# Kernel optimization log

Hardware: AMD Instinct MI355X
Metric: run time of the kernel (lower is better)

## Reference

```python
import jax, jax.numpy as jnp
import numpy as np

H = 256          # hidden_size
W2V = 256        # word2vec embedding dim
FEAT = 4096      # video frame feature dim
T_ENC = 80       # video_frame


def _lstm_cell(x, h, c, W_ih, W_hh, b_ih, b_hh):
    # PyTorch LSTMCell gate order: i, f, g, o
    gates = x @ W_ih.T + b_ih + h @ W_hh.T + b_hh
    i, f, g, o = jnp.split(gates, 4, axis=-1)
    c_new = jax.nn.sigmoid(f) * c + jax.nn.sigmoid(i) * jnp.tanh(g)
    h_new = jax.nn.sigmoid(o) * jnp.tanh(c_new)
    return h_new, c_new


def setup_inputs() -> dict:
    key = jax.random.key(0)
    ks = jax.random.split(key, 14)
    B, L, V = 256, 40, 6000
    sc = 0.02
    inp = {
        "feat": jax.random.normal(ks[0], (B, T_ENC, FEAT), jnp.float32),
        "caption": jax.random.normal(ks[1], (B, L, W2V), jnp.float32),
        "caption_one_hot": jax.random.normal(ks[2], (B, L, V), jnp.float32),
        # lstm1: input 4096 -> hidden 256
        "W_ih1": jax.random.normal(ks[3], (4 * H, FEAT), jnp.float32) * sc,
        "W_hh1": jax.random.normal(ks[4], (4 * H, H), jnp.float32) * sc,
        "b_ih1": jnp.zeros((4 * H,), jnp.float32),
        "b_hh1": jnp.zeros((4 * H,), jnp.float32),
        # lstm2: input hidden+word2vec = 512 -> hidden 256
        "W_ih2": jax.random.normal(ks[5], (4 * H, H + W2V), jnp.float32) * sc,
        "W_hh2": jax.random.normal(ks[6], (4 * H, H), jnp.float32) * sc,
        "b_ih2": jnp.zeros((4 * H,), jnp.float32),
        "b_hh2": jnp.zeros((4 * H,), jnp.float32),
        # output projection hidden -> vocab
        "W_out": jax.random.normal(ks[7], (V, H), jnp.float32) * sc,
        "b_out": jnp.zeros((V,), jnp.float32),
    }
    return inp


def reference(feat, caption, caption_one_hot,
              W_ih1, W_hh1, b_ih1, b_hh1,
              W_ih2, W_hh2, b_ih2, b_hh2,
              W_out, b_out):
    B = feat.shape[0]
    L = caption.shape[1]  # decoder_length
    pad1 = jnp.zeros((B, FEAT), feat.dtype)
    pad2 = jnp.zeros((B, H), feat.dtype)
    h1 = jnp.zeros((B, H), feat.dtype)
    c1 = jnp.zeros((B, H), feat.dtype)
    h2 = jnp.zeros((B, H), feat.dtype)
    c2 = jnp.zeros((B, H), feat.dtype)

    # ---- encoding phase: 80 video frames ----
    def enc_step(carry, x_t):
        h1, c1, h2, c2 = carry
        h1, c1 = _lstm_cell(x_t, h1, c1, W_ih1, W_hh1, b_ih1, b_hh1)
        h2, c2 = _lstm_cell(jnp.concatenate([pad2, h1], axis=1), h2, c2,
                            W_ih2, W_hh2, b_ih2, b_hh2)
        return (h1, c1, h2, c2), None

    carry, _ = jax.lax.scan(enc_step, (h1, c1, h2, c2),
                            feat.transpose(1, 0, 2))  # [T,B,4096]

    # ---- decoding phase: decoder_length-1 steps with per-step CE ----
    targets = jnp.argmax(caption_one_hot, axis=-1)      # [B,L] int
    dec_in = caption[:, :L - 1, :].transpose(1, 0, 2)   # [L-1,B,W2V]
    dec_tgt = targets[:, 1:].T                          # [L-1,B]

    def dec_step(carry, xt):
        h1, c1, h2, c2 = carry
        cap_t, tgt_t = xt
        h1, c1 = _lstm_cell(pad1, h1, c1, W_ih1, W_hh1, b_ih1, b_hh1)
        h2, c2 = _lstm_cell(jnp.concatenate([cap_t, h1], axis=1), h2, c2,
                            W_ih2, W_hh2, b_ih2, b_hh2)
        logits = h2 @ W_out.T + b_out                   # [B,V]
        lsm = jax.nn.log_softmax(logits, axis=-1)
        nll = -jnp.take_along_axis(lsm, tgt_t[:, None], axis=1)[:, 0]
        # torch: total_loss += sum(word_loss)/batch_size  ==  mean over batch
        return (h1, c1, h2, c2), jnp.mean(nll)

    _, step_losses = jax.lax.scan(dec_step, carry, (dec_in, dec_tgt))
    return jnp.sum(step_losses)
```

## Files before the change

kernel.cpp:

```cpp
#include <hip/hip_runtime.h>


typedef unsigned short u16;
typedef __attribute__((ext_vector_type(8))) short s8v;
typedef __attribute__((ext_vector_type(4))) float f4v;

#define VOC   6000
#define VOCP  6016
#define CHUNK_M 3328

__device__ __forceinline__ u16 f2b(float f) {
  unsigned u = __float_as_uint(f);
  unsigned r = (u + 0x7fffu + ((u >> 16) & 1u)) >> 16;
  return (u16)r;
}
__device__ __forceinline__ float sigm(float x) { return 1.f / (1.f + __expf(-x)); }
__device__ __forceinline__ float tanh_f(float x) {
  float e = __expf(-2.f * fabsf(x));
  float t = (1.f - e) / (1.f + e);
  return x >= 0.f ? t : -t;
}

__global__ void pack_bf16(u16* __restrict__ dst, int dld, int doff,
                          const float* __restrict__ src, int sld, int soff,
                          int Wc, int R, int Rsrc) {
  int i = blockIdx.x * 256 + threadIdx.x;
  if (i >= Wc * R) return;
  int r = i / Wc, c = i - r * Wc;
  float v = (r < Rsrc) ? src[(size_t)r * sld + soff + c] : 0.f;
  dst[(size_t)r * dld + doff + c] = f2b(v);
}

__global__ void bias_setup(const float* __restrict__ bi1, const float* __restrict__ bh1,
                           const float* __restrict__ bi2, const float* __restrict__ bh2,
                           const float* __restrict__ bo,
                           float* __restrict__ b1s, float* __restrict__ b2s,
                           float* __restrict__ bop) {
  int i = blockIdx.x * 256 + threadIdx.x;
  if (i < 1024) { b1s[i] = bi1[i] + bh1[i]; b2s[i] = bi2[i] + bh2[i]; }
  if (i < VOCP) bop[i] = (i < VOC) ? bo[i] : 0.f;
}

__global__ __launch_bounds__(256) void argmax_kernel(const float* __restrict__ coh,
                                                     int* __restrict__ tgt) {
  const int d = blockIdx.x >> 8;
  const int b = blockIdx.x & 255;
  const float* row = coh + ((size_t)b * 40 + (d + 1)) * VOC;
  float best = -3.4e38f; int bi = 0;
  for (int n = threadIdx.x; n < VOC; n += 256) {
    float v = row[n];
    if (v > best) { best = v; bi = n; }
  }
#pragma unroll
  for (int o = 1; o < 64; o <<= 1) {
    float ov = __shfl_xor(best, o);
    int   oi = __shfl_xor(bi, o);
    if (ov > best || (ov == best && oi < bi)) { best = ov; bi = oi; }
  }
  __shared__ float sv[4]; __shared__ int si[4];
  if ((threadIdx.x & 63) == 0) { sv[threadIdx.x >> 6] = best; si[threadIdx.x >> 6] = bi; }
  __syncthreads();
  if (threadIdx.x == 0) {
    for (int i = 1; i < 4; ++i)
      if (sv[i] > best || (sv[i] == best && si[i] < bi)) { best = sv[i]; bi = si[i]; }
    tgt[blockIdx.x] = bi;
  }
}

__global__ __launch_bounds__(256) void gemm_bf16(
    const float* __restrict__ A, const u16* __restrict__ Bw,
    const float* __restrict__ bias, float* __restrict__ C,
    int K, int lda, int ldc)
{
  const int n0 = blockIdx.x * 128;
  const int m0 = blockIdx.y * 128;
  const int tid = threadIdx.x;
  const int lane = tid & 63;
  const int wid = tid >> 6;
  const int wm = wid >> 1, wn = wid & 1;
  const int fr = lane & 15;
  const int fk = (lane >> 4) * 8;
  const int sr = tid >> 1;
  const int sc = (tid & 1) * 32;

  __shared__ u16 As[128][72];
  __shared__ u16 Bs[128][72];
  f4v acc[4][4] = {};

  for (int k0 = 0; k0 < K; k0 += 64) {
    const float* ap = A + (size_t)(m0 + sr) * lda + (k0 + sc);
    const u16*   bp = Bw + (size_t)(n0 + sr) * K + (k0 + sc);
    float af[32];
#pragma unroll
    for (int v = 0; v < 8; ++v) {
      float4 t4 = *reinterpret_cast<const float4*>(ap + v * 4);
      af[v*4+0] = t4.x; af[v*4+1] = t4.y; af[v*4+2] = t4.z; af[v*4+3] = t4.w;
    }
    int4 bv[4];
#pragma unroll
    for (int v = 0; v < 4; ++v) bv[v] = *reinterpret_cast<const int4*>(bp + v * 8);
    __syncthreads();
#pragma unroll
    for (int v = 0; v < 4; ++v) {
      int w0 = (int)((unsigned)f2b(af[v*8+0]) | ((unsigned)f2b(af[v*8+1]) << 16));
      int w1 = (int)((unsigned)f2b(af[v*8+2]) | ((unsigned)f2b(af[v*8+3]) << 16));
      int w2 = (int)((unsigned)f2b(af[v*8+4]) | ((unsigned)f2b(af[v*8+5]) << 16));
      int w3 = (int)((unsigned)f2b(af[v*8+6]) | ((unsigned)f2b(af[v*8+7]) << 16));
      *reinterpret_cast<int4*>(&As[sr][sc + v*8]) = make_int4(w0, w1, w2, w3);
      *reinterpret_cast<int4*>(&Bs[sr][sc + v*8]) = bv[v];
    }
    __syncthreads();
#pragma unroll
    for (int ks = 0; ks < 2; ++ks) {
      const int kb = ks * 32 + fk;
      s8v a[4], b[4];
#pragma unroll
      for (int i = 0; i < 4; ++i)
        a[i] = *reinterpret_cast<const s8v*>(&As[wm*64 + i*16 + fr][kb]);
#pragma unroll
      for (int j = 0; j < 4; ++j)
        b[j] = *reinterpret_cast<const s8v*>(&Bs[wn*64 + j*16 + fr][kb]);
#pragma unroll
      for (int i = 0; i < 4; ++i)
#pragma unroll
        for (int j = 0; j < 4; ++j)
          acc[i][j] = __builtin_amdgcn_mfma_f32_16x16x32_bf16(a[i], b[j], acc[i][j], 0, 0, 0);
    }
  }
#pragma unroll
  for (int j = 0; j < 4; ++j) {
    const int n = n0 + wn*64 + j*16 + fr;
    const float bz = bias[n];
#pragma unroll
    for (int i = 0; i < 4; ++i) {
      const int rb = m0 + wm*64 + i*16 + (lane >> 4) * 4;
#pragma unroll
      for (int r = 0; r < 4; ++r)
        C[(size_t)(rb + r) * ldc + n] = acc[i][j][r] + bz;
    }
  }
}

__global__ __launch_bounds__(256) void step_kernel(
    int t,
    const float* __restrict__ X1,
    const float* __restrict__ Xc,
    const float* __restrict__ b1sum, const float* __restrict__ b2sum,
    const u16* __restrict__ Whh1,
    const u16* __restrict__ Wcat2,
    u16* __restrict__ hcat, float* __restrict__ c1, float* __restrict__ c2,
    float* __restrict__ H2dec)
{
  const int lane = threadIdx.x & 63;
  const int w = threadIdx.x >> 6;
  const int fr = lane & 15;
  const int fk = (lane >> 4) * 8;
  const u16* hr = hcat + (size_t)((t + 1) & 1) * (256 * 512);
  u16*       hw = hcat + (size_t)(t & 1) * (256 * 512);

  if (blockIdx.x < 64) {
    if (t > 118) return;
    const int bm = blockIdx.x >> 4;
    const int bh = blockIdx.x & 15;
    const int rowbase = bm * 64 + w * 16;
    f4v acc[4] = {};
    const u16* arow = hr + (size_t)(rowbase + fr) * 512;
#pragma unroll
    for (int kk = 0; kk < 8; ++kk) {
      const int kb = kk * 32 + fk;
      s8v a = *reinterpret_cast<const s8v*>(arow + kb);
#pragma unroll
      for (int q = 0; q < 4; ++q) {
        s8v wv = *reinterpret_cast<const s8v*>(Whh1 + (size_t)(q*256 + bh*16 + fr) * 256 + kb);
        acc[q] = __builtin_amdgcn_mfma_f32_16x16x32_bf16(a, wv, acc[q], 0, 0, 0);
      }
    }
    const int hd = bh * 16 + fr;
    float xb0 = 0, xb1 = 0, xb2 = 0, xb3 = 0;
    if (t >= 80) { xb0 = b1sum[hd]; xb1 = b1sum[256+hd]; xb2 = b1sum[512+hd]; xb3 = b1sum[768+hd]; }
#pragma unroll
    for (int r = 0; r < 4; ++r) {
      const int bat = rowbase + (lane >> 4) * 4 + r;
      float g0 = acc[0][r], g1 = acc[1][r], g2 = acc[2][r], g3 = acc[3][r];
      if (t < 80) {
        const float* xp = X1 + ((size_t)bat * 80 + t) * 1024;
        g0 += xp[hd]; g1 += xp[256+hd]; g2 += xp[512+hd]; g3 += xp[768+hd];
      } else { g0 += xb0; g1 += xb1; g2 += xb2; g3 += xb3; }
      const int ci = bat * 256 + hd;
      float co = c1[ci];
      float ii = sigm(g0), ff = sigm(g1), gg = tanh_f(g2), oo = sigm(g3);
      float cn = ff * co + ii * gg;
      float h = oo * tanh_f(cn);
      c1[ci] = cn;
      hw[(size_t)bat * 512 + hd] = f2b(h);
    }
  } else {
    if (t < 1) return;
    const int s = t - 1;
    const int bb = blockIdx.x - 64;
    const int bm = bb >> 4;
    const int bh = bb & 15;
    const int rowbase = bm * 64 + w * 16;
    f4v acc[4] = {};
    const u16* arow = hr + (size_t)(rowbase + fr) * 512;
#pragma unroll
    for (int kk = 0; kk < 16; ++kk) {
      const int kb = kk * 32 + fk;
      s8v a = *reinterpret_cast<const s8v*>(arow + kb);
#pragma unroll
      for (int q = 0; q < 4; ++q) {
        s8v wv = *reinterpret_cast<const s8v*>(Wcat2 + (size_t)(q*256 + bh*16 + fr) * 512 + kb);
        acc[q] = __builtin_amdgcn_mfma_f32_16x16x32_bf16(a, wv, acc[q], 0, 0, 0);
      }
    }
    const int hd = bh * 16 + fr;
    float xb0 = 0, xb1 = 0, xb2 = 0, xb3 = 0;
    if (s < 80) { xb0 = b2sum[hd]; xb1 = b2sum[256+hd]; xb2 = b2sum[512+hd]; xb3 = b2sum[768+hd]; }
#pragma unroll
    for (int r = 0; r < 4; ++r) {
      const int bat = rowbase + (lane >> 4) * 4 + r;
      float g0 = acc[0][r], g1 = acc[1][r], g2 = acc[2][r], g3 = acc[3][r];
      if (s >= 80) {
        const float* xp = Xc + ((size_t)bat * 40 + (s - 80)) * 1024;
        g0 += xp[hd]; g1 += xp[256+hd]; g2 += xp[512+hd]; g3 += xp[768+hd];
      } else { g0 += xb0; g1 += xb1; g2 += xb2; g3 += xb3; }
      const int ci = bat * 256 + hd;
      float co = c2[ci];
      float ii = sigm(g0), ff = sigm(g1), gg = tanh_f(g2), oo = sigm(g3);
      float cn = ff * co + ii * gg;
      float h = oo * tanh_f(cn);
      c2[ci] = cn;
      hw[(size_t)bat * 512 + 256 + hd] = f2b(h);
      if (s >= 80) H2dec[((size_t)(s - 80) * 256 + bat) * 256 + hd] = h;
    }
  }
}

__global__ __launch_bounds__(256) void nll_kernel(const float* __restrict__ logits,
                                                  const int* __restrict__ tgt,
                                                  float* __restrict__ rowloss, int rg0) {
  const int rl = blockIdx.x;
  const float* row = logits + (size_t)rl * VOCP;
  const int tid = threadIdx.x;
  float mx = -3.4e38f;
  for (int n = tid; n < VOC; n += 256) mx = fmaxf(mx, row[n]);
#pragma unroll
  for (int o = 1; o < 64; o <<= 1) mx = fmaxf(mx, __shfl_xor(mx, o));
  __shared__ float s1[4];
  if ((tid & 63) == 0) s1[tid >> 6] = mx;
  __syncthreads();
  mx = fmaxf(fmaxf(s1[0], s1[1]), fmaxf(s1[2], s1[3]));
  float sm = 0.f;
  for (int n = tid; n < VOC; n += 256) sm += __expf(row[n] - mx);
#pragma unroll
  for (int o = 1; o < 64; o <<= 1) sm += __shfl_xor(sm, o);
  __shared__ float s2[4];
  if ((tid & 63) == 0) s2[tid >> 6] = sm;
  __syncthreads();
  if (tid == 0) {
    float tot = s2[0] + s2[1] + s2[2] + s2[3];
    rowloss[rg0 + rl] = mx + __logf(tot) - row[tgt[rg0 + rl]];
  }
}

__global__ __launch_bounds__(256) void final_kernel(const float* __restrict__ rowloss,
                                                    float* __restrict__ out) {
  float s = 0.f;
  for (int n = threadIdx.x; n < 9984; n += 256) s += rowloss[n];
#pragma unroll
  for (int o = 1; o < 64; o <<= 1) s += __shfl_xor(s, o);
  __shared__ float sr[4];
  if ((threadIdx.x & 63) == 0) sr[threadIdx.x >> 6] = s;
  __syncthreads();
  if (threadIdx.x == 0) out[0] = (sr[0] + sr[1] + sr[2] + sr[3]) * (1.f / 256.f);
}

extern "C" void kernel_launch(void* const* d_in, const int* in_sizes, int n_in,
                              void* d_out, int out_size, void* d_ws, size_t ws_size,
                              hipStream_t stream) {
  const float* feat    = (const float*)d_in[0];
  const float* caption = (const float*)d_in[1];
  const float* coh     = (const float*)d_in[2];
  const float* W_ih1   = (const float*)d_in[3];
  const float* W_hh1   = (const float*)d_in[4];
  const float* b_ih1   = (const float*)d_in[5];
  const float* b_hh1   = (const float*)d_in[6];
  const float* W_ih2   = (const float*)d_in[7];
  const float* W_hh2   = (const float*)d_in[8];
  const float* b_ih2   = (const float*)d_in[9];
  const float* b_hh2   = (const float*)d_in[10];
  const float* W_out   = (const float*)d_in[11];
  const float* b_out   = (const float*)d_in[12];

  char* p = (char*)d_ws;
  auto take = [&](size_t bytes) { char* r = p; p += (bytes + 255) & ~(size_t)255; return r; };
  float* X1     = (float*)take(20480ull * 1024 * 4);
  float* Xc     = (float*)take(10240ull * 1024 * 4);
  float* H2dec  = (float*)take(9984ull * 256 * 4);
  float* logits = (float*)take((size_t)CHUNK_M * VOCP * 4);
  u16* Wih1b  = (u16*)take(1024ull * 4096 * 2);
  u16* Whh1b  = (u16*)take(1024ull * 256 * 2);
  u16* Wih2ab = (u16*)take(1024ull * 256 * 2);
  u16* Wcat2b = (u16*)take(1024ull * 512 * 2);
  u16* Woutb  = (u16*)take((size_t)VOCP * 256 * 2);
  u16* hcat   = (u16*)take(2ull * 256 * 512 * 2);
  float* c1   = (float*)take(256ull * 256 * 4);
  float* c2   = (float*)take(256ull * 256 * 4);
  float* b1sum = (float*)take(1024 * 4);
  float* b2sum = (float*)take(1024 * 4);
  float* boutp = (float*)take(VOCP * 4);
  int*   tgt   = (int*)take(9984 * 4);
  float* rowloss = (float*)take(9984 * 4);

  hipMemsetAsync(hcat, 0, 2ull * 256 * 512 * 2 + 2ull * 256 * 256 * 4, stream);
  bias_setup<<<dim3(24), dim3(256), 0, stream>>>(b_ih1, b_hh1, b_ih2, b_hh2, b_out,
                                                 b1sum, b2sum, boutp);
  auto pack = [&](u16* dst, int dld, int doff, const float* src, int sld, int soff,
                  int Wc, int R, int Rs) {
    int tot = Wc * R;
    pack_bf16<<<dim3((tot + 255) / 256), dim3(256), 0, stream>>>(dst, dld, doff, src, sld, soff,
                                                                 Wc, R, Rs);
  };
  pack(Wih1b, 4096, 0, W_ih1, 4096, 0, 4096, 1024, 1024);
  pack(Whh1b, 256, 0, W_hh1, 256, 0, 256, 1024, 1024);
  pack(Wih2ab, 256, 0, W_ih2, 512, 0, 256, 1024, 1024);
  pack(Wcat2b, 512, 0, W_ih2, 512, 256, 256, 1024, 1024);
  pack(Wcat2b, 512, 256, W_hh2, 256, 0, 256, 1024, 1024);
  pack(Woutb, 256, 0, W_out, 256, 0, 256, VOCP, VOC);

  argmax_kernel<<<dim3(39 * 256), dim3(256), 0, stream>>>(coh, tgt);

  gemm_bf16<<<dim3(8, 160), dim3(256), 0, stream>>>(feat, Wih1b, b1sum, X1, 4096, 4096, 1024);
  gemm_bf16<<<dim3(8, 80), dim3(256), 0, stream>>>(caption, Wih2ab, b2sum, Xc, 256, 256, 1024);

  for (int t = 0; t <= 119; ++t)
    step_kernel<<<dim3(128), dim3(256), 0, stream>>>(t, X1, Xc, b1sum, b2sum,
                                                     Whh1b, Wcat2b, hcat, c1, c2, H2dec);

  for (int ch = 0; ch < 3; ++ch) {
    gemm_bf16<<<dim3(VOCP / 128, CHUNK_M / 128), dim3(256), 0, stream>>>(
        H2dec + (size_t)ch * CHUNK_M * 256, Woutb, boutp, logits, 256, 256, VOCP);
    nll_kernel<<<dim3(CHUNK_M), dim3(256), 0, stream>>>(logits, tgt, rowloss, ch * CHUNK_M);
  }
  final_kernel<<<dim3(1), dim3(256), 0, stream>>>(rowloss, (float*)d_out);
}
```

Measured before the change: 2.717 ms.

## Persistent recurrent kernel with grid barrier, bf16 intermediates, larger GEMM tiles

Replaces the 120 per-step launches with one persistent kernel. It keeps recurrent weights and cell state in registers and synchronises steps through a global atomic barrier. Feature and caption inputs are converted to bf16 in a separate pass, and the GEMM becomes a 128x256 tile with register prefetch of the next K slice. X1, Xc and H2dec are now stored in bf16, and argmax/nll use vectorised loads. This cuts launch overhead and memory traffic, but the spin barrier needs all 128 blocks co-resident, and the extra bf16 rounding may shift numerics.

```diff
diff --git a/kernel.cpp b/kernel.cpp
--- a/kernel.cpp
+++ b/kernel.cpp
@@ -6,19 +6,36 @@
 typedef __attribute__((ext_vector_type(4))) float f4v;
 
 #define VOC   6000
-#define VOCP  6016
+#define VOCP  6144
 #define CHUNK_M 3328
 
 __device__ __forceinline__ u16 f2b(float f) {
   unsigned u = __float_as_uint(f);
   unsigned r = (u + 0x7fffu + ((u >> 16) & 1u)) >> 16;
   return (u16)r;
+}
+__device__ __forceinline__ float b2f(u16 u) {
+  return __uint_as_float(((unsigned)u) << 16);
 }
 __device__ __forceinline__ float sigm(float x) { return 1.f / (1.f + __expf(-x)); }
 __device__ __forceinline__ float tanh_f(float x) {
   float e = __expf(-2.f * fabsf(x));
   float t = (1.f - e) / (1.f + e);
   return x >= 0.f ? t : -t;
+}
+
+__global__ __launch_bounds__(256) void conv_f2b(const float* __restrict__ src,
+                                                u16* __restrict__ dst, long n) {
+  long stride = (long)gridDim.x * 2048;
+  for (long i = ((long)blockIdx.x * 256 + threadIdx.x) * 8; i < n; i += stride) {
+    float4 a = *(const float4*)(src + i);
+    float4 b = *(const float4*)(src + i + 4);
+    unsigned w0 = (unsigned)f2b(a.x) | ((unsigned)f2b(a.y) << 16);
+    unsigned w1 = (unsigned)f2b(a.z) | ((unsigned)f2b(a.w) << 16);
+    unsigned w2 = (unsigned)f2b(b.x) | ((unsigned)f2b(b.y) << 16);
+    unsigned w3 = (unsigned)f2b(b.z) | ((unsigned)f2b(b.w) << 16);
+    *(int4*)(dst + i) = make_int4((int)w0, (int)w1, (int)w2, (int)w3);
+  }
 }
 
 __global__ void pack_bf16(u16* __restrict__ dst, int dld, int doff,
@@ -45,11 +62,14 @@
                                                      int* __restrict__ tgt) {
   const int d = blockIdx.x >> 8;
   const int b = blockIdx.x & 255;
-  const float* row = coh + ((size_t)b * 40 + (d + 1)) * VOC;
+  const float4* row = (const float4*)(coh + ((size_t)b * 40 + (d + 1)) * VOC);
   float best = -3.4e38f; int bi = 0;
-  for (int n = threadIdx.x; n < VOC; n += 256) {
-    float v = row[n];
-    if (v > best) { best = v; bi = n; }
+  for (int v = threadIdx.x; v < VOC / 4; v += 256) {
+    float4 x = row[v];
+    float vals[4] = {x.x, x.y, x.z, x.w};
+#pragma unroll
+    for (int j = 0; j < 4; ++j)
+      if (vals[j] > best) { best = vals[j]; bi = v * 4 + j; }
   }
 #pragma unroll
   for (int o = 1; o < 64; o <<= 1) {
@@ -67,172 +87,225 @@
   }
 }
 
-__global__ __launch_bounds__(256) void gemm_bf16(
-    const float* __restrict__ A, const u16* __restrict__ Bw,
-    const float* __restrict__ bias, float* __restrict__ C,
-    int K, int lda, int ldc)
+template <int OB>
+__global__ __launch_bounds__(256) void gemm_bb(
+    const u16* __restrict__ A, const u16* __restrict__ Bw,
+    const float* __restrict__ bias, void* __restrict__ Cout,
+    int K, int ldc)
 {
-  const int n0 = blockIdx.x * 128;
-  const int m0 = blockIdx.y * 128;
+  const int m0 = blockIdx.x * 128;
+  const int n0 = blockIdx.y * 256;
   const int tid = threadIdx.x;
   const int lane = tid & 63;
   const int wid = tid >> 6;
   const int wm = wid >> 1, wn = wid & 1;
   const int fr = lane & 15;
   const int fk = (lane >> 4) * 8;
-  const int sr = tid >> 1;
-  const int sc = (tid & 1) * 32;
+  const int rq = lane >> 4;
 
   __shared__ u16 As[128][72];
-  __shared__ u16 Bs[128][72];
-  f4v acc[4][4] = {};
-
+  __shared__ u16 Bs[256][72];
+  f4v acc[4][8] = {};
+
+  const int ar = tid >> 1, ac = (tid & 1) * 32;
+  int4 av[4], bv[8];
+  {
+    const u16* ap = A + (size_t)(m0 + ar) * K + ac;
+    const u16* bp = Bw + (size_t)(n0 + tid) * K;
+#pragma unroll
+    for (int v = 0; v < 4; ++v) av[v] = *(const int4*)(ap + v * 8);
+#pragma unroll
+    for (int v = 0; v < 8; ++v) bv[v] = *(const int4*)(bp + v * 8);
+  }
+#pragma unroll 1
   for (int k0 = 0; k0 < K; k0 += 64) {
-    const float* ap = A + (size_t)(m0 + sr) * lda + (k0 + sc);
-    const u16*   bp = Bw + (size_t)(n0 + sr) * K + (k0 + sc);
-    float af[32];
-#pragma unroll
-    for (int v = 0; v < 8; ++v) {
-      float4 t4 = *reinterpret_cast<const float4*>(ap + v * 4);
-      af[v*4+0] = t4.x; af[v*4+1] = t4.y; af[v*4+2] = t4.z; af[v*4+3] = t4.w;
-    }
-    int4 bv[4];
-#pragma unroll
-    for (int v = 0; v < 4; ++v) bv[v] = *reinterpret_cast<const int4*>(bp + v * 8);
     __syncthreads();
 #pragma unroll
-    for (int v = 0; v < 4; ++v) {
-      int w0 = (int)((unsigned)f2b(af[v*8+0]) | ((unsigned)f2b(af[v*8+1]) << 16));
-      int w1 = (int)((unsigned)f2b(af[v*8+2]) | ((unsigned)f2b(af[v*8+3]) << 16));
-      int w2 = (int)((unsigned)f2b(af[v*8+4]) | ((unsigned)f2b(af[v*8+5]) << 16));
-      int w3 = (int)((unsigned)f2b(af[v*8+6]) | ((unsigned)f2b(af[v*8+7]) << 16));
-      *reinterpret_cast<int4*>(&As[sr][sc + v*8]) = make_int4(w0, w1, w2, w3);
-      *reinterpret_cast<int4*>(&Bs[sr][sc + v*8]) = bv[v];
-    }
+    for (int v = 0; v < 4; ++v) *(int4*)&As[ar][ac + v * 8] = av[v];
+#pragma unroll
+    for (int v = 0; v < 8; ++v) *(int4*)&Bs[tid][v * 8] = bv[v];
     __syncthreads();
+    if (k0 + 64 < K) {
+      const u16* ap = A + (size_t)(m0 + ar) * K + k0 + 64 + ac;
+      const u16* bp = Bw + (size_t)(n0 + tid) * K + k0 + 64;
+#pragma unroll
+      for (int v = 0; v < 4; ++v) av[v] = *(const int4*)(ap + v * 8);
+#pragma unroll
+      for (int v = 0; v < 8; ++v) bv[v] = *(const int4*)(bp + v * 8);
+    }
 #pragma unroll
     for (int ks = 0; ks < 2; ++ks) {
       const int kb = ks * 32 + fk;
-      s8v a[4], b[4];
+      s8v a[4], b[8];
+#pragma unroll
+      for (int i = 0; i < 4; ++i) a[i] = *(const s8v*)&As[wm * 64 + i * 16 + fr][kb];
+#pragma unroll
+      for (int j = 0; j < 8; ++j) b[j] = *(const s8v*)&Bs[wn * 128 + j * 16 + fr][kb];
 #pragma unroll
       for (int i = 0; i < 4; ++i)
-        a[i] = *reinterpret_cast<const s8v*>(&As[wm*64 + i*16 + fr][kb]);
-#pragma unroll
-      for (int j = 0; j < 4; ++j)
-        b[j] = *reinterpret_cast<const s8v*>(&Bs[wn*64 + j*16 + fr][kb]);
-#pragma unroll
-      for (int i = 0; i < 4; ++i)
-#pragma unroll
-        for (int j = 0; j < 4; ++j)
+#pragma unroll
+        for (int j = 0; j < 8; ++j)
           acc[i][j] = __builtin_amdgcn_mfma_f32_16x16x32_bf16(a[i], b[j], acc[i][j], 0, 0, 0);
     }
   }
 #pragma unroll
-  for (int j = 0; j < 4; ++j) {
-    const int n = n0 + wn*64 + j*16 + fr;
+  for (int j = 0; j < 8; ++j) {
+    const int n = n0 + wn * 128 + j * 16 + fr;
     const float bz = bias[n];
 #pragma unroll
     for (int i = 0; i < 4; ++i) {
-      const int rb = m0 + wm*64 + i*16 + (lane >> 4) * 4;
-#pragma unroll
-      for (int r = 0; r < 4; ++r)
-        C[(size_t)(rb + r) * ldc + n] = acc[i][j][r] + bz;
-    }
-  }
-}
-
-__global__ __launch_bounds__(256) void step_kernel(
-    int t,
-    const float* __restrict__ X1,
-    const float* __restrict__ Xc,
+      const int rb = m0 + wm * 64 + i * 16 + rq * 4;
+#pragma unroll
+      for (int r = 0; r < 4; ++r) {
+        float vout = acc[i][j][r] + bz;
+        if (OB) ((u16*)Cout)[(size_t)(rb + r) * ldc + n] = f2b(vout);
+        else    ((float*)Cout)[(size_t)(rb + r) * ldc + n] = vout;
+      }
+    }
+  }
+}
+
+__device__ __forceinline__ void gbar(unsigned* bar, unsigned target) {
+  __syncthreads();
+  if (threadIdx.x == 0) {
+    __threadfence();
+    __hip_atomic_fetch_add(bar, 1u, __ATOMIC_RELEASE, __HIP_MEMORY_SCOPE_AGENT);
+    while (__hip_atomic_load(bar, __ATOMIC_RELAXED, __HIP_MEMORY_SCOPE_AGENT) < target) {
+      __builtin_amdgcn_s_sleep(2);
+    }
+    __threadfence();
+  }
+  __syncthreads();
+}
+
+__global__ __launch_bounds__(256, 1) void recur_kernel(
+    const u16* __restrict__ X1,
+    const u16* __restrict__ Xc,
     const float* __restrict__ b1sum, const float* __restrict__ b2sum,
     const u16* __restrict__ Whh1,
     const u16* __restrict__ Wcat2,
-    u16* __restrict__ hcat, float* __restrict__ c1, float* __restrict__ c2,
-    float* __restrict__ H2dec)
+    u16* __restrict__ hcat,
+    u16* __restrict__ H2dec,
+    unsigned* __restrict__ bar)
 {
-  const int lane = threadIdx.x & 63;
-  const int w = threadIdx.x >> 6;
+  const int tid = threadIdx.x;
+  const int lane = tid & 63;
+  const int w = tid >> 6;
   const int fr = lane & 15;
   const int fk = (lane >> 4) * 8;
-  const u16* hr = hcat + (size_t)((t + 1) & 1) * (256 * 512);
-  u16*       hw = hcat + (size_t)(t & 1) * (256 * 512);
-
-  if (blockIdx.x < 64) {
-    if (t > 118) return;
-    const int bm = blockIdx.x >> 4;
-    const int bh = blockIdx.x & 15;
-    const int rowbase = bm * 64 + w * 16;
-    f4v acc[4] = {};
-    const u16* arow = hr + (size_t)(rowbase + fr) * 512;
-#pragma unroll
-    for (int kk = 0; kk < 8; ++kk) {
-      const int kb = kk * 32 + fk;
-      s8v a = *reinterpret_cast<const s8v*>(arow + kb);
-#pragma unroll
-      for (int q = 0; q < 4; ++q) {
-        s8v wv = *reinterpret_cast<const s8v*>(Whh1 + (size_t)(q*256 + bh*16 + fr) * 256 + kb);
-        acc[q] = __builtin_amdgcn_mfma_f32_16x16x32_bf16(a, wv, acc[q], 0, 0, 0);
+  const int rq = lane >> 4;
+  const bool p2 = blockIdx.x >= 64;
+  const int bb = p2 ? (int)blockIdx.x - 64 : (int)blockIdx.x;
+  const int bm = bb >> 4;
+  const int bh = bb & 15;
+  const int hd = bh * 16 + fr;
+  const int rowA = bm * 64 + w * 16 + fr;
+  const int batbase = bm * 64 + w * 16 + rq * 4;
+
+  s8v wv[64];
+  float br[4];
+  if (!p2) {
+#pragma unroll
+    for (int q = 0; q < 4; ++q) {
+      br[q] = b1sum[q * 256 + hd];
+#pragma unroll
+      for (int kk = 0; kk < 8; ++kk)
+        wv[q * 8 + kk] =
+            *(const s8v*)(Whh1 + (size_t)(q * 256 + bh * 16 + fr) * 256 + kk * 32 + fk);
+    }
+  } else {
+#pragma unroll
+    for (int q = 0; q < 4; ++q) {
+      br[q] = b2sum[q * 256 + hd];
+#pragma unroll
+      for (int kk = 0; kk < 16; ++kk)
+        wv[q * 16 + kk] =
+            *(const s8v*)(Wcat2 + (size_t)(q * 256 + bh * 16 + fr) * 512 + kk * 32 + fk);
+    }
+  }
+  float creg[4] = {0.f, 0.f, 0.f, 0.f};
+
+#pragma unroll 1
+  for (int t = 0; t < 120; ++t) {
+    const u16* hr = hcat + (size_t)((t + 1) & 1) * (256 * 512);
+    u16* hw = hcat + (size_t)(t & 1) * (256 * 512);
+    if (!p2) {
+      if (t <= 118) {
+        float ga[4][4];
+        if (t < 80) {
+#pragma unroll
+          for (int r = 0; r < 4; ++r) {
+            const u16* xp = X1 + ((size_t)(batbase + r) * 80 + t) * 1024;
+#pragma unroll
+            for (int q = 0; q < 4; ++q) ga[r][q] = b2f(xp[q * 256 + hd]);
+          }
+        } else {
+#pragma unroll
+          for (int r = 0; r < 4; ++r)
+#pragma unroll
+            for (int q = 0; q < 4; ++q) ga[r][q] = br[q];
+        }
+        f4v acc[4] = {};
+        const u16* arow = hr + (size_t)rowA * 512;
+#pragma unroll
+        for (int kk = 0; kk < 8; ++kk) {
+          s8v a = *(const s8v*)(arow + kk * 32 + fk);
+#pragma unroll
+          for (int q = 0; q < 4; ++q)
+            acc[q] = __builtin_amdgcn_mfma_f32_16x16x32_bf16(a, wv[q * 8 + kk], acc[q], 0, 0, 0);
+        }
+#pragma unroll
+        for (int r = 0; r < 4; ++r) {
+          const int bat = batbase + r;
+          float g0 = acc[0][r] + ga[r][0], g1 = acc[1][r] + ga[r][1];
+          float g2 = acc[2][r] + ga[r][2], g3 = acc[3][r] + ga[r][3];
+          float cn = sigm(g1) * creg[r] + sigm(g0) * tanh_f(g2);
+          float h = sigm(g3) * tanh_f(cn);
+          creg[r] = cn;
+          hw[(size_t)bat * 512 + hd] = f2b(h);
+        }
       }
-    }
-    const int hd = bh * 16 + fr;
-    float xb0 = 0, xb1 = 0, xb2 = 0, xb3 = 0;
-    if (t >= 80) { xb0 = b1sum[hd]; xb1 = b1sum[256+hd]; xb2 = b1sum[512+hd]; xb3 = b1sum[768+hd]; }
-#pragma unroll
-    for (int r = 0; r < 4; ++r) {
-      const int bat = rowbase + (lane >> 4) * 4 + r;
-      float g0 = acc[0][r], g1 = acc[1][r], g2 = acc[2][r], g3 = acc[3][r];
-      if (t < 80) {
-        const float* xp = X1 + ((size_t)bat * 80 + t) * 1024;
-        g0 += xp[hd]; g1 += xp[256+hd]; g2 += xp[512+hd]; g3 += xp[768+hd];
-      } else { g0 += xb0; g1 += xb1; g2 += xb2; g3 += xb3; }
-      const int ci = bat * 256 + hd;
-      float co = c1[ci];
-      float ii = sigm(g0), ff = sigm(g1), gg = tanh_f(g2), oo = sigm(g3);
-      float cn = ff * co + ii * gg;
-      float h = oo * tanh_f(cn);
-      c1[ci] = cn;
-      hw[(size_t)bat * 512 + hd] = f2b(h);
-    }
-  } else {
-    if (t < 1) return;
-    const int s = t - 1;
-    const int bb = blockIdx.x - 64;
-    const int bm = bb >> 4;
-    const int bh = bb & 15;
-    const int rowbase = bm * 64 + w * 16;
-    f4v acc[4] = {};
-    const u16* arow = hr + (size_t)(rowbase + fr) * 512;
-#pragma unroll
-    for (int kk = 0; kk < 16; ++kk) {
-      const int kb = kk * 32 + fk;
-      s8v a = *reinterpret_cast<const s8v*>(arow + kb);
-#pragma unroll
-      for (int q = 0; q < 4; ++q) {
-        s8v wv = *reinterpret_cast<const s8v*>(Wcat2 + (size_t)(q*256 + bh*16 + fr) * 512 + kb);
-        acc[q] = __builtin_amdgcn_mfma_f32_16x16x32_bf16(a, wv, acc[q], 0, 0, 0);
+    } else {
+      if (t >= 1) {
+        const int s = t - 1;
+        float ga[4][4];
+        if (s >= 80) {
+#pragma unroll
+          for (int r = 0; r < 4; ++r) {
+            const u16* xp = Xc + ((size_t)(batbase + r) * 40 + (s - 80)) * 1024;
+#pragma unroll
+            for (int q = 0; q < 4; ++q) ga[r][q] = b2f(xp[q * 256 + hd]);
+          }
+        } else {
+#pragma unroll
+          for (int r = 0; r < 4; ++r)
+#pragma unroll
+            for (int q = 0; q < 4; ++q) ga[r][q] = br[q];
+        }
+        f4v acc[4] = {};
+        const u16* arow = hr + (size_t)rowA * 512;
+#pragma unroll
+        for (int kk = 0; kk < 16; ++kk) {
+          s8v a = *(const s8v*)(arow + kk * 32 + fk);
+#pragma unroll
+          for (int q = 0; q < 4; ++q)
+            acc[q] = __builtin_amdgcn_mfma_f32_16x16x32_bf16(a, wv[q * 16 + kk], acc[q], 0, 0, 0);
+        }
+#pragma unroll
+        for (int r = 0; r < 4; ++r) {
+          const int bat = batbase + r;
+          float g0 = acc[0][r] + ga[r][0], g1 = acc[1][r] + ga[r][1];
+          float g2 = acc[2][r] + ga[r][2], g3 = acc[3][r] + ga[r][3];
+          float cn = sigm(g1) * creg[r] + sigm(g0) * tanh_f(g2);
+          float h = sigm(g3) * tanh_f(cn);
+          creg[r] = cn;
+          u16 hb = f2b(h);
+          hw[(size_t)bat * 512 + 256 + hd] = hb;
+          if (s >= 80) H2dec[((size_t)(s - 80) * 256 + bat) * 256 + hd] = hb;
+        }
       }
     }
-    const int hd = bh * 16 + fr;
-    float xb0 = 0, xb1 = 0, xb2 = 0, xb3 = 0;
-    if (s < 80) { xb0 = b2sum[hd]; xb1 = b2sum[256+hd]; xb2 = b2sum[512+hd]; xb3 = b2sum[768+hd]; }
-#pragma unroll
-    for (int r = 0; r < 4; ++r) {
-      const int bat = rowbase + (lane >> 4) * 4 + r;
-      float g0 = acc[0][r], g1 = acc[1][r], g2 = acc[2][r], g3 = acc[3][r];
-      if (s >= 80) {
-        const float* xp = Xc + ((size_t)bat * 40 + (s - 80)) * 1024;
-        g0 += xp[hd]; g1 += xp[256+hd]; g2 += xp[512+hd]; g3 += xp[768+hd];
-      } else { g0 += xb0; g1 += xb1; g2 += xb2; g3 += xb3; }
-      const int ci = bat * 256 + hd;
-      float co = c2[ci];
-      float ii = sigm(g0), ff = sigm(g1), gg = tanh_f(g2), oo = sigm(g3);
-      float cn = ff * co + ii * gg;
-      float h = oo * tanh_f(cn);
-      c2[ci] = cn;
-      hw[(size_t)bat * 512 + 256 + hd] = f2b(h);
-      if (s >= 80) H2dec[((size_t)(s - 80) * 256 + bat) * 256 + hd] = h;
-    }
+    if (t < 119) gbar(bar, 128u * (unsigned)(t + 1));
   }
 }
 
@@ -241,9 +314,13 @@
                                                   float* __restrict__ rowloss, int rg0) {
   const int rl = blockIdx.x;
   const float* row = logits + (size_t)rl * VOCP;
+  const float4* row4 = (const float4*)row;
   const int tid = threadIdx.x;
   float mx = -3.4e38f;
-  for (int n = tid; n < VOC; n += 256) mx = fmaxf(mx, row[n]);
+  for (int v = tid; v < VOC / 4; v += 256) {
+    float4 x = row4[v];
+    mx = fmaxf(mx, fmaxf(fmaxf(x.x, x.y), fmaxf(x.z, x.w)));
+  }
 #pragma unroll
   for (int o = 1; o < 64; o <<= 1) mx = fmaxf(mx, __shfl_xor(mx, o));
   __shared__ float s1[4];
@@ -251,7 +328,10 @@
   __syncthreads();
   mx = fmaxf(fmaxf(s1[0], s1[1]), fmaxf(s1[2], s1[3]));
   float sm = 0.f;
-  for (int n = tid; n < VOC; n += 256) sm += __expf(row[n] - mx);
+  for (int v = tid; v < VOC / 4; v += 256) {
+    float4 x = row4[v];
+    sm += __expf(x.x - mx) + __expf(x.y - mx) + __expf(x.z - mx) + __expf(x.w - mx);
+  }
 #pragma unroll
   for (int o = 1; o < 64; o <<= 1) sm += __shfl_xor(sm, o);
   __shared__ float s2[4];
@@ -294,25 +374,29 @@
 
   char* p = (char*)d_ws;
   auto take = [&](size_t bytes) { char* r = p; p += (bytes + 255) & ~(size_t)255; return r; };
-  float* X1     = (float*)take(20480ull * 1024 * 4);
-  float* Xc     = (float*)take(10240ull * 1024 * 4);
-  float* H2dec  = (float*)take(9984ull * 256 * 4);
-  float* logits = (float*)take((size_t)CHUNK_M * VOCP * 4);
+  u16* X1b    = (u16*)take(20480ull * 1024 * 2);
+  u16* Xcb    = (u16*)take(10240ull * 1024 * 2);
   u16* Wih1b  = (u16*)take(1024ull * 4096 * 2);
   u16* Whh1b  = (u16*)take(1024ull * 256 * 2);
   u16* Wih2ab = (u16*)take(1024ull * 256 * 2);
   u16* Wcat2b = (u16*)take(1024ull * 512 * 2);
   u16* Woutb  = (u16*)take((size_t)VOCP * 256 * 2);
   u16* hcat   = (u16*)take(2ull * 256 * 512 * 2);
-  float* c1   = (float*)take(256ull * 256 * 4);
-  float* c2   = (float*)take(256ull * 256 * 4);
   float* b1sum = (float*)take(1024 * 4);
   float* b2sum = (float*)take(1024 * 4);
   float* boutp = (float*)take(VOCP * 4);
   int*   tgt   = (int*)take(9984 * 4);
   float* rowloss = (float*)take(9984 * 4);
-
-  hipMemsetAsync(hcat, 0, 2ull * 256 * 512 * 2 + 2ull * 256 * 256 * 4, stream);
+  unsigned* bar  = (unsigned*)take(256);
+  char* uni = p;
+  u16* featb = (u16*)uni;
+  u16* capb  = (u16*)(uni + 10240ull * 4096 * 2);
+  u16* H2dec = (u16*)uni;
+  float* logits = (float*)(uni + ((9984ull * 256 * 2 + 255) & ~(size_t)255));
+
+  hipMemsetAsync(hcat, 0, 2ull * 256 * 512 * 2, stream);
+  hipMemsetAsync(bar, 0, 4, stream);
+
   bias_setup<<<dim3(24), dim3(256), 0, stream>>>(b_ih1, b_hh1, b_ih2, b_hh2, b_out,
                                                  b1sum, b2sum, boutp);
   auto pack = [&](u16* dst, int dld, int doff, const float* src, int sld, int soff,
@@ -330,16 +414,23 @@
 
   argmax_kernel<<<dim3(39 * 256), dim3(256), 0, stream>>>(coh, tgt);
 
-  gemm_bf16<<<dim3(8, 160), dim3(256), 0, stream>>>(feat, Wih1b, b1sum, X1, 4096, 4096, 1024);
-  gemm_bf16<<<dim3(8, 80), dim3(256), 0, stream>>>(caption, Wih2ab, b2sum, Xc, 256, 256, 1024);
-
-  for (int t = 0; t <= 119; ++t)
-    step_kernel<<<dim3(128), dim3(256), 0, stream>>>(t, X1, Xc, b1sum, b2sum,
-                                                     Whh1b, Wcat2b, hcat, c1, c2, H2dec);
+  conv_f2b<<<dim3(2048), dim3(256), 0, stream>>>(caption, capb, 10240L * 256);
+  gemm_bb<1><<<dim3(80, 4), dim3(256), 0, stream>>>(capb, Wih2ab, b2sum, Xcb, 256, 1024);
+
+  for (int c = 0; c < 2; ++c) {
+    conv_f2b<<<dim3(2048), dim3(256), 0, stream>>>(feat + (size_t)c * 10240 * 4096, featb,
+                                                   10240L * 4096);
+    gemm_bb<1><<<dim3(80, 4), dim3(256), 0, stream>>>(featb, Wih1b, b1sum,
+                                                      X1b + (size_t)c * 10240 * 1024,
+                                                      4096, 1024);
+  }
+
+  recur_kernel<<<dim3(128), dim3(256), 0, stream>>>(X1b, Xcb, b1sum, b2sum,
+                                                    Whh1b, Wcat2b, hcat, H2dec, bar);
 
   for (int ch = 0; ch < 3; ++ch) {
-    gemm_bf16<<<dim3(VOCP / 128, CHUNK_M / 128), dim3(256), 0, stream>>>(
-        H2dec + (size_t)ch * CHUNK_M * 256, Woutb, boutp, logits, 256, 256, VOCP);
+    gemm_bb<0><<<dim3(CHUNK_M / 128, VOCP / 256), dim3(256), 0, stream>>>(
+        H2dec + (size_t)ch * CHUNK_M * 256, Woutb, boutp, logits, 256, VOCP);
     nll_kernel<<<dim3(CHUNK_M), dim3(256), 0, stream>>>(logits, tgt, rowloss, ch * CHUNK_M);
   }
   final_kernel<<<dim3(1), dim3(256), 0, stream>>>(rowloss, (float*)d_out);
```

After: 3.287 ms. 1.21x slower.
